# Kernel tuning notes

Hardware: AMD Instinct MI355X
Metric: run time of the kernel (lower is better)

## Reference

```python
import jax, jax.numpy as jnp
import numpy as np

D_THRESH = 0.5  # init arg `dist`


def setup_inputs() -> dict:
    key = jax.random.key(0)
    k1, k2 = jax.random.split(key)
    N, M, C = 20000, 25000, 3
    pointcloud = jax.random.uniform(k1, (N, C), dtype=jnp.float32)
    pointcloud_padding = jax.random.uniform(k2, (M, C), dtype=jnp.float32)
    return {"pointcloud": pointcloud, "pointcloud_padding": pointcloud_padding}


def reference(pointcloud, pointcloud_padding):
    # torch.cdist(padding, pointcloud): Euclidean distance matrix [M, N]
    # via the GEMM formulation ||a||^2 + ||b||^2 - 2 a.b (matches torch's path)
    a2 = jnp.sum(pointcloud_padding * pointcloud_padding, axis=1)[:, None]  # [M,1]
    b2 = jnp.sum(pointcloud * pointcloud, axis=1)[None, :]                  # [1,N]
    ab = pointcloud_padding @ pointcloud.T                                  # [M,N]
    dist = jnp.sqrt(jnp.maximum(a2 + b2 - 2.0 * ab, 0.0))                   # [M,N]
    # count neighbors within radius, per pointcloud point
    counts = jnp.sum(dist <= D_THRESH, axis=0).astype(jnp.int32)            # [N]
    out = counts.reshape(-1, 1)[: pointcloud.shape[0]]                      # [N,1]
    return out
```

## Files before the change

kernel.cpp:

```cpp
#include <hip/hip_runtime.h>

typedef short  bf16x8 __attribute__((ext_vector_type(8)));

#define JS      8
#define STREAMS (JS * 4)
#define TI      128

__device__ __forceinline__ unsigned short f2bf(float x) {
    unsigned u = __builtin_bit_cast(unsigned, x);
    u += 0x7FFF + ((u >> 16) & 1);
    return (unsigned short)(u >> 16);
}
__device__ __forceinline__ float bf2f(unsigned short h) {
    unsigned u = ((unsigned)h) << 16;
    return __builtin_bit_cast(float, u);
}

__global__ __launch_bounds__(256) void dens_pack_kernel(
    const float* __restrict__ pad, uint4* __restrict__ ws,
    int* __restrict__ out, int M, int mtot, int N)
{
    const int j = blockIdx.x * 256 + threadIdx.x;
    if (j < N) out[j] = 0;
    if (j >= mtot) return;

    float qx = 0.f, qy = 0.f, qz = 0.f;
    float negc = -1.0e6f;
    if (j < M) {
        qx = pad[3 * j]; qy = pad[3 * j + 1]; qz = pad[3 * j + 2];
        negc = 0.125f - 0.5f * (qx * qx + qy * qy + qz * qz);
    }
    const unsigned short xh = f2bf(qx), yh = f2bf(qy), zh = f2bf(qz);
    const unsigned short xl = f2bf(qx - bf2f(xh));
    const unsigned short yl = f2bf(qy - bf2f(yh));
    const unsigned short zl = f2bf(qz - bf2f(zh));
    const unsigned short ch = f2bf(negc);
    const unsigned short cl = f2bf(negc - bf2f(ch));

    uint4 p0, p1;
    p0.x = (unsigned)xh | ((unsigned)yh << 16);
    p0.y = (unsigned)zh | ((unsigned)xl << 16);
    p0.z = (unsigned)yl | ((unsigned)zl << 16);
    p0.w = (unsigned)xh | ((unsigned)yh << 16);
    p1.x = (unsigned)zh | ((unsigned)xl << 16);
    p1.y = (unsigned)yl | ((unsigned)zl << 16);
    p1.z = (unsigned)ch | ((unsigned)cl << 16);
    p1.w = 0;
    ws[j]        = p0;
    ws[mtot + j] = p1;
}

__device__ __forceinline__ void make_bfrag(const float* __restrict__ pc,
                                           int i, int N, int half,
                                           bf16x8& B, float& ha)
{
    float px = 0.f, py = 0.f, pz = 0.f;
    ha = 3.0e38f;
    if (i < N) {
        px = pc[3 * i]; py = pc[3 * i + 1]; pz = pc[3 * i + 2];
        ha = 0.5f * (px * px + py * py + pz * pz);
    }
    const short xh = (short)f2bf(px), yh = (short)f2bf(py), zh = (short)f2bf(pz);
    const short xl = (short)f2bf(px - bf2f((unsigned short)xh));
    const short yl = (short)f2bf(py - bf2f((unsigned short)yh));
    const short zl = (short)f2bf(pz - bf2f((unsigned short)zh));
    const short ONE = (short)0x3F80;
    const bf16x8 B0 = {xh, yh, zh, xh, yh, zh, xl, yl};
    const bf16x8 B1 = {zl, xl, yl, zl, ONE, ONE, 0, 0};
    B = half ? B1 : B0;
}

#define CONSUME(R, HA, CC) \
    "v_cmp_le_f32 vcc, " HA ", " R "\n\t" \
    "v_addc_co_u32 " CC ", vcc, 0, " CC ", vcc\n\t"
#define CONS4(R0, R1, R2, R3, HA, CC) \
    CONSUME(R0, HA, CC) CONSUME(R1, HA, CC) CONSUME(R2, HA, CC) CONSUME(R3, HA, CC)

__global__ __launch_bounds__(256, 2) void dens_mfma_kernel(
    const float* __restrict__ pc,
    const char*  __restrict__ wsA,
    int* __restrict__ out,
    int N, int jt, int p1off)
{
    const int lane = threadIdx.x & 63;
    const int w    = threadIdx.x >> 6;
    const int n    = lane & 31;
    const int half = lane >> 5;

    const int ibase = blockIdx.x * TI;
    bf16x8 B0, B1, B2, B3; float ha0, ha1, ha2, ha3;
    make_bfrag(pc, ibase + n,      N, half, B0, ha0);
    make_bfrag(pc, ibase + 32 + n, N, half, B1, ha1);
    make_bfrag(pc, ibase + 64 + n, N, half, B2, ha2);
    make_bfrag(pc, ibase + 96 + n, N, half, B3, ha3);

    const int stream = blockIdx.y * 4 + w;
    const unsigned long long a0 =
        (unsigned long long)(wsA + (half ? p1off : 0) + n * 16 + (size_t)stream * 512);
    const unsigned alo = (unsigned)a0;
    const unsigned ahi = (unsigned)(a0 >> 32);

    int visits = (jt + STREAMS - 1) / STREAMS;
    int c0 = 0, c1 = 0, c2 = 0, c3 = 0;

    asm volatile(
        "v_mov_b32 v88, %13\n\t"
        "v_mov_b32 v89, %14\n\t"
        "v_mov_b32 v64, 0\n\t" "v_mov_b32 v65, 0\n\t"
        "v_mov_b32 v66, 0\n\t" "v_mov_b32 v67, 0\n\t"
        "v_mov_b32 v68, 0\n\t" "v_mov_b32 v69, 0\n\t"
        "v_mov_b32 v70, 0\n\t" "v_mov_b32 v71, 0\n\t"
        "v_mov_b32 v72, 0\n\t" "v_mov_b32 v73, 0\n\t"
        "v_mov_b32 v74, 0\n\t" "v_mov_b32 v75, 0\n\t"
        "v_mov_b32 v76, 0\n\t" "v_mov_b32 v77, 0\n\t"
        "v_mov_b32 v78, 0\n\t" "v_mov_b32 v79, 0\n\t"
        "global_load_dwordx4 v[84:87], v[88:89], off\n\t"
        "v_add_co_u32 v88, vcc, 0x4000, v88\n\t"
        "v_addc_co_u32 v89, vcc, 0, v89, vcc\n\t"
        "Ldens%=:\n\t"
        "s_waitcnt vmcnt(0)\n\t"
        "v_mov_b32 v80, v84\n\t"
        "v_mov_b32 v81, v85\n\t"
        "v_mov_b32 v82, v86\n\t"
        "v_mov_b32 v83, v87\n\t"
        "global_load_dwordx4 v[84:87], v[88:89], off\n\t"
        "v_add_co_u32 v88, vcc, 0x4000, v88\n\t"
        "v_addc_co_u32 v89, vcc, 0, v89, vcc\n\t"
        "v_mfma_f32_32x32x16_bf16 v[32:47], v[80:83], %5, v[64:79]\n\t"
        "v_mfma_f32_32x32x16_bf16 v[48:63], v[80:83], %6, v[64:79]\n\t"
        "s_nop 7\n\t"
        "s_nop 2\n\t"
        CONS4("v32","v33","v34","v35","%9","%0")
        CONS4("v36","v37","v38","v39","%9","%0")
        CONS4("v40","v41","v42","v43","%9","%0")
        CONS4("v44","v45","v46","v47","%9","%0")
        "v_mfma_f32_32x32x16_bf16 v[32:47], v[80:83], %7, v[64:79]\n\t"
        CONS4("v48","v49","v50","v51","%10","%1")
        CONS4("v52","v53","v54","v55","%10","%1")
        CONS4("v56","v57","v58","v59","%10","%1")
        CONS4("v60","v61","v62","v63","%10","%1")
        "v_mfma_f32_32x32x16_bf16 v[48:63], v[80:83], %8, v[64:79]\n\t"
        CONS4("v32","v33","v34","v35","%11","%2")
        CONS4("v36","v37","v38","v39","%11","%2")
        CONS4("v40","v41","v42","v43","%11","%2")
        CONS4("v44","v45","v46","v47","%11","%2")
        CONS4("v48","v49","v50","v51","%12","%3")
        CONS4("v52","v53","v54","v55","%12","%3")
        CONS4("v56","v57","v58","v59","%12","%3")
        CONS4("v60","v61","v62","v63","%12","%3")
        "s_sub_u32 %4, %4, 1\n\t"
        "s_cmp_lg_u32 %4, 0\n\t"
        "s_cbranch_scc1 Ldens%=\n\t"
        : "+v"(c0), "+v"(c1), "+v"(c2), "+v"(c3), "+s"(visits)
        : "v"(B0), "v"(B1), "v"(B2), "v"(B3),
          "v"(ha0), "v"(ha1), "v"(ha2), "v"(ha3),
          "v"(alo), "v"(ahi)
        : "vcc", "scc", "memory",
          "v32","v33","v34","v35","v36","v37","v38","v39",
          "v40","v41","v42","v43","v44","v45","v46","v47",
          "v48","v49","v50","v51","v52","v53","v54","v55",
          "v56","v57","v58","v59","v60","v61","v62","v63",
          "v64","v65","v66","v67","v68","v69","v70","v71",
          "v72","v73","v74","v75","v76","v77","v78","v79",
          "v80","v81","v82","v83","v84","v85","v86","v87",
          "v88","v89");

    int g0 = c0 + __shfl_xor(c0, 32);
    int g1 = c1 + __shfl_xor(c1, 32);
    int g2 = c2 + __shfl_xor(c2, 32);
    int g3 = c3 + __shfl_xor(c3, 32);

    __shared__ int red[4][TI];
    if (lane < 32) {
        red[w][n]      = g0;
        red[w][n + 32] = g1;
        red[w][n + 64] = g2;
        red[w][n + 96] = g3;
    }
    __syncthreads();
    if (threadIdx.x < TI) {
        const int ii = ibase + threadIdx.x;
        if (ii < N) {
            const int s = red[0][threadIdx.x] + red[1][threadIdx.x] +
                          red[2][threadIdx.x] + red[3][threadIdx.x];
            atomicAdd(&out[ii], s);
        }
    }
}

extern "C" void kernel_launch(void* const* d_in, const int* in_sizes, int n_in,
                              void* d_out, int out_size, void* d_ws, size_t ws_size,
                              hipStream_t stream) {
    const float* pc  = (const float*)d_in[0];
    const float* pad = (const float*)d_in[1];
    int* out = (int*)d_out;

    const int N = in_sizes[0] / 3;
    const int M = in_sizes[1] / 3;
    const int jt     = (M + 31) / 32;
    const int visits = (jt + STREAMS - 1) / STREAMS;
    const int jtp    = (visits + 1) * STREAMS;
    const int mtot   = jtp * 32;

    dens_pack_kernel<<<(mtot + 255) / 256, 256, 0, stream>>>(
        pad, (uint4*)d_ws, out, M, mtot, N);

    dim3 grid((N + TI - 1) / TI, JS);
    dens_mfma_kernel<<<grid, 256, 0, stream>>>(
        pc, (const char*)d_ws, out, N, jt, mtot * 16);
}
```

Baseline: 91.85 us.

## Double-buffer A loads, split compare accumulators, raise occupancy and grid split

Unrolls the main loop by two visits and keeps two A-fragment registers, each with its own address stream, so a load is always in flight and the register copy is gone. Compare results go to separate SGPR pairs with split counters, which breaks the vcc dependency chain between the compare and add-with-carry steps. Launch bounds rise to four blocks per CU and the M split grows from 8 to 13 stream groups to give the machine more parallel work. The padded workspace and the visit count are adjusted to match. The risks are a clash with the hardcoded SGPR numbers and the extra register pressure.

```diff
diff --git a/kernel.cpp b/kernel.cpp
--- a/kernel.cpp
+++ b/kernel.cpp
@@ -2,7 +2,7 @@
 
 typedef short  bf16x8 __attribute__((ext_vector_type(8)));
 
-#define JS      8
+#define JS      13
 #define STREAMS (JS * 4)
 #define TI      128
 
@@ -70,17 +70,57 @@
     B = half ? B1 : B0;
 }
 
-#define CONSUME(R, HA, CC) \
-    "v_cmp_le_f32 vcc, " HA ", " R "\n\t" \
-    "v_addc_co_u32 " CC ", vcc, 0, " CC ", vcc\n\t"
-#define CONS4(R0, R1, R2, R3, HA, CC) \
-    CONSUME(R0, HA, CC) CONSUME(R1, HA, CC) CONSUME(R2, HA, CC) CONSUME(R3, HA, CC)
-
-__global__ __launch_bounds__(256, 2) void dens_mfma_kernel(
+#define CSLICE(R0, R1, R2, R3, HA, CA, CB) \
+    "v_cmp_le_f32 s[60:61], " HA ", " R0 "\n\t" \
+    "v_cmp_le_f32 s[62:63], " HA ", " R1 "\n\t" \
+    "v_cmp_le_f32 s[64:65], " HA ", " R2 "\n\t" \
+    "v_cmp_le_f32 s[66:67], " HA ", " R3 "\n\t" \
+    "v_addc_co_u32 " CA ", s[60:61], 0, " CA ", s[60:61]\n\t" \
+    "v_addc_co_u32 " CB ", s[62:63], 0, " CB ", s[62:63]\n\t" \
+    "v_addc_co_u32 " CA ", s[64:65], 0, " CA ", s[64:65]\n\t" \
+    "v_addc_co_u32 " CB ", s[66:67], 0, " CB ", s[66:67]\n\t"
+
+#define CGRP(B0R,B1R,B2R,B3R, B4R,B5R,B6R,B7R, B8R,B9R,BAR,BBR, BCR,BDR,BER,BFR, HA, CA, CB) \
+    CSLICE(B0R,B1R,B2R,B3R, HA, CA, CB) \
+    CSLICE(B4R,B5R,B6R,B7R, HA, CA, CB) \
+    CSLICE(B8R,B9R,BAR,BBR, HA, CA, CB) \
+    CSLICE(BCR,BDR,BER,BFR, HA, CA, CB)
+
+#define CONS_D0(HA, CA, CB) \
+    CGRP("v32","v33","v34","v35","v36","v37","v38","v39", \
+         "v40","v41","v42","v43","v44","v45","v46","v47", HA, CA, CB)
+#define CONS_D1(HA, CA, CB) \
+    CGRP("v48","v49","v50","v51","v52","v53","v54","v55", \
+         "v56","v57","v58","v59","v60","v61","v62","v63", HA, CA, CB)
+
+#define VISIT(AR, AD) \
+    "s_waitcnt vmcnt(1)\n\t" \
+    "v_mfma_f32_32x32x16_bf16 v[32:47], " AR ", %9,  v[64:79]\n\t" \
+    "v_mfma_f32_32x32x16_bf16 v[48:63], " AR ", %10, v[64:79]\n\t" \
+    "s_nop 7\n\t" \
+    "s_nop 2\n\t" \
+    CONS_D0("%13", "%0", "%1") \
+    "v_mfma_f32_32x32x16_bf16 v[32:47], " AR ", %11, v[64:79]\n\t" \
+    CONS_D1("%14", "%2", "%3") \
+    "v_mfma_f32_32x32x16_bf16 v[48:63], " AR ", %12, v[64:79]\n\t" \
+    "global_load_dwordx4 " AR ", " AD ", off\n\t" \
+    "v_add_co_u32 " AD##_LO ", vcc, 0xd000, " AD##_LO "\n\t" \
+    "v_addc_co_u32 " AD##_HI ", vcc, 0, " AD##_HI ", vcc\n\t" \
+    CONS_D0("%15", "%4", "%5") \
+    CONS_D1("%16", "%6", "%7")
+
+#define ADX "v[88:89]"
+#define ADX_LO "v88"
+#define ADX_HI "v89"
+#define ADY "v[90:91]"
+#define ADY_LO "v90"
+#define ADY_HI "v91"
+
+__global__ __launch_bounds__(256, 4) void dens_mfma_kernel(
     const float* __restrict__ pc,
     const char*  __restrict__ wsA,
     int* __restrict__ out,
-    int N, int jt, int p1off)
+    int N, int iters, int p1off)
 {
     const int lane = threadIdx.x & 63;
     const int w    = threadIdx.x >> 6;
@@ -95,17 +135,20 @@
     make_bfrag(pc, ibase + 96 + n, N, half, B3, ha3);
 
     const int stream = blockIdx.y * 4 + w;
-    const unsigned long long a0 =
+    const unsigned long long ax =
         (unsigned long long)(wsA + (half ? p1off : 0) + n * 16 + (size_t)stream * 512);
-    const unsigned alo = (unsigned)a0;
-    const unsigned ahi = (unsigned)(a0 >> 32);
-
-    int visits = (jt + STREAMS - 1) / STREAMS;
-    int c0 = 0, c1 = 0, c2 = 0, c3 = 0;
+    const unsigned long long ay = ax + STREAMS * 512;
+    const unsigned xlo = (unsigned)ax, xhi = (unsigned)(ax >> 32);
+    const unsigned ylo = (unsigned)ay, yhi = (unsigned)(ay >> 32);
+
+    int it = iters;
+    int c0a = 0, c0b = 0, c1a = 0, c1b = 0, c2a = 0, c2b = 0, c3a = 0, c3b = 0;
 
     asm volatile(
-        "v_mov_b32 v88, %13\n\t"
-        "v_mov_b32 v89, %14\n\t"
+        "v_mov_b32 v88, %17\n\t"
+        "v_mov_b32 v89, %18\n\t"
+        "v_mov_b32 v90, %19\n\t"
+        "v_mov_b32 v91, %20\n\t"
         "v_mov_b32 v64, 0\n\t" "v_mov_b32 v65, 0\n\t"
         "v_mov_b32 v66, 0\n\t" "v_mov_b32 v67, 0\n\t"
         "v_mov_b32 v68, 0\n\t" "v_mov_b32 v69, 0\n\t"
@@ -114,48 +157,25 @@
         "v_mov_b32 v74, 0\n\t" "v_mov_b32 v75, 0\n\t"
         "v_mov_b32 v76, 0\n\t" "v_mov_b32 v77, 0\n\t"
         "v_mov_b32 v78, 0\n\t" "v_mov_b32 v79, 0\n\t"
-        "global_load_dwordx4 v[84:87], v[88:89], off\n\t"
-        "v_add_co_u32 v88, vcc, 0x4000, v88\n\t"
+        "global_load_dwordx4 v[80:83], v[88:89], off\n\t"
+        "v_add_co_u32 v88, vcc, 0xd000, v88\n\t"
         "v_addc_co_u32 v89, vcc, 0, v89, vcc\n\t"
+        "global_load_dwordx4 v[84:87], v[90:91], off\n\t"
+        "v_add_co_u32 v90, vcc, 0xd000, v90\n\t"
+        "v_addc_co_u32 v91, vcc, 0, v91, vcc\n\t"
         "Ldens%=:\n\t"
-        "s_waitcnt vmcnt(0)\n\t"
-        "v_mov_b32 v80, v84\n\t"
-        "v_mov_b32 v81, v85\n\t"
-        "v_mov_b32 v82, v86\n\t"
-        "v_mov_b32 v83, v87\n\t"
-        "global_load_dwordx4 v[84:87], v[88:89], off\n\t"
-        "v_add_co_u32 v88, vcc, 0x4000, v88\n\t"
-        "v_addc_co_u32 v89, vcc, 0, v89, vcc\n\t"
-        "v_mfma_f32_32x32x16_bf16 v[32:47], v[80:83], %5, v[64:79]\n\t"
-        "v_mfma_f32_32x32x16_bf16 v[48:63], v[80:83], %6, v[64:79]\n\t"
-        "s_nop 7\n\t"
-        "s_nop 2\n\t"
-        CONS4("v32","v33","v34","v35","%9","%0")
-        CONS4("v36","v37","v38","v39","%9","%0")
-        CONS4("v40","v41","v42","v43","%9","%0")
-        CONS4("v44","v45","v46","v47","%9","%0")
-        "v_mfma_f32_32x32x16_bf16 v[32:47], v[80:83], %7, v[64:79]\n\t"
-        CONS4("v48","v49","v50","v51","%10","%1")
-        CONS4("v52","v53","v54","v55","%10","%1")
-        CONS4("v56","v57","v58","v59","%10","%1")
-        CONS4("v60","v61","v62","v63","%10","%1")
-        "v_mfma_f32_32x32x16_bf16 v[48:63], v[80:83], %8, v[64:79]\n\t"
-        CONS4("v32","v33","v34","v35","%11","%2")
-        CONS4("v36","v37","v38","v39","%11","%2")
-        CONS4("v40","v41","v42","v43","%11","%2")
-        CONS4("v44","v45","v46","v47","%11","%2")
-        CONS4("v48","v49","v50","v51","%12","%3")
-        CONS4("v52","v53","v54","v55","%12","%3")
-        CONS4("v56","v57","v58","v59","%12","%3")
-        CONS4("v60","v61","v62","v63","%12","%3")
-        "s_sub_u32 %4, %4, 1\n\t"
-        "s_cmp_lg_u32 %4, 0\n\t"
+        VISIT("v[80:83]", ADX)
+        VISIT("v[84:87]", ADY)
+        "s_sub_u32 %8, %8, 1\n\t"
+        "s_cmp_lg_u32 %8, 0\n\t"
         "s_cbranch_scc1 Ldens%=\n\t"
-        : "+v"(c0), "+v"(c1), "+v"(c2), "+v"(c3), "+s"(visits)
+        : "+v"(c0a), "+v"(c0b), "+v"(c1a), "+v"(c1b),
+          "+v"(c2a), "+v"(c2b), "+v"(c3a), "+v"(c3b), "+s"(it)
         : "v"(B0), "v"(B1), "v"(B2), "v"(B3),
           "v"(ha0), "v"(ha1), "v"(ha2), "v"(ha3),
-          "v"(alo), "v"(ahi)
+          "v"(xlo), "v"(xhi), "v"(ylo), "v"(yhi)
         : "vcc", "scc", "memory",
+          "s60","s61","s62","s63","s64","s65","s66","s67",
           "v32","v33","v34","v35","v36","v37","v38","v39",
           "v40","v41","v42","v43","v44","v45","v46","v47",
           "v48","v49","v50","v51","v52","v53","v54","v55",
@@ -163,12 +183,12 @@
           "v64","v65","v66","v67","v68","v69","v70","v71",
           "v72","v73","v74","v75","v76","v77","v78","v79",
           "v80","v81","v82","v83","v84","v85","v86","v87",
-          "v88","v89");
-
-    int g0 = c0 + __shfl_xor(c0, 32);
-    int g1 = c1 + __shfl_xor(c1, 32);
-    int g2 = c2 + __shfl_xor(c2, 32);
-    int g3 = c3 + __shfl_xor(c3, 32);
+          "v88","v89","v90","v91");
+
+    int g0 = (c0a + c0b); g0 += __shfl_xor(g0, 32);
+    int g1 = (c1a + c1b); g1 += __shfl_xor(g1, 32);
+    int g2 = (c2a + c2b); g2 += __shfl_xor(g2, 32);
+    int g3 = (c3a + c3b); g3 += __shfl_xor(g3, 32);
 
     __shared__ int red[4][TI];
     if (lane < 32) {
@@ -197,15 +217,16 @@
 
     const int N = in_sizes[0] / 3;
     const int M = in_sizes[1] / 3;
-    const int jt     = (M + 31) / 32;
-    const int visits = (jt + STREAMS - 1) / STREAMS;
-    const int jtp    = (visits + 1) * STREAMS;
-    const int mtot   = jtp * 32;
+    const int jt = (M + 31) / 32;
+    int visits = (jt + STREAMS - 1) / STREAMS;
+    if (visits & 1) visits++;
+    const int jtp  = (visits + 2) * STREAMS;
+    const int mtot = jtp * 32;
 
     dens_pack_kernel<<<(mtot + 255) / 256, 256, 0, stream>>>(
         pad, (uint4*)d_ws, out, M, mtot, N);
 
     dim3 grid((N + TI - 1) / TI, JS);
     dens_mfma_kernel<<<grid, 256, 0, stream>>>(
-        pc, (const char*)d_ws, out, N, jt, mtot * 16);
-}
+        pc, (const char*)d_ws, out, N, visits / 2, mtot * 16);
+}
```

Measured after the change: 93.52 us. About the same (+1.8%).
